# Kernel optimization log

Measured on AMD Instinct MI355X. Metric: run time of the kernel, lower is better.

## Reference

```python
import jax, jax.numpy as jnp
import numpy as np


def setup_inputs() -> dict:
    key = jax.random.key(0)
    ks = jax.random.split(key, 6)
    B, H, W, C = 4, 64, 64, 256
    D = 256 // 4  # inter_channel // 4
    return {
        "g": jax.random.normal(ks[0], (B, H, W, C), dtype=jnp.float32),
        "x": jax.random.normal(ks[1], (B, H, W, C), dtype=jnp.float32),
        "x_query": jax.random.normal(ks[2], (B, H, W, D), dtype=jnp.float32),
        "phi_g": jax.random.normal(ks[3], (B, H, W, D), dtype=jnp.float32),
        "x_value": jax.random.normal(ks[4], (B, H, W, C), dtype=jnp.float32),
        "k": jax.random.normal(ks[5], (1,), dtype=jnp.float32),
    }


def reference(g, x, x_query, phi_g, x_value, k):
    B, H, W, C = x.shape
    D = x_query.shape[-1]
    HW = H * W
    q = x_query.reshape(B, HW, D)
    pg = phi_g.reshape(B, HW, D)
    v = x_value.reshape(B, HW, C)
    # scale[b,i,j] = sum_d phi_g[b,i,d] * x_query[b,j,d]  -> (B, HW, HW)
    scale = jnp.einsum("bid,bjd->bij", pg, q)
    soft = jax.nn.softmax(scale, axis=-1)
    # scaled_value[b,i,c] = sum_j soft[b,i,j] * v[b,j,c]
    sv = jnp.einsum("bij,bjc->bic", soft, v).reshape(B, H, W, C)
    layero = k * sv + x
    return jnp.concatenate([layero, g], axis=3)
```

## Files before the change

kernel.cpp:

```cpp
#include <hip/hip_runtime.h>

#define N_  4096
#define D_  64
#define C_  256

typedef short bf16x8 __attribute__((ext_vector_type(8)));
typedef float f32x4  __attribute__((ext_vector_type(4)));

__device__ __forceinline__ unsigned short f2bf(float f) {
    union { float f; unsigned int i; } v; v.f = f;
    unsigned int r = v.i + 0x7fffu + ((v.i >> 16) & 1u);
    return (unsigned short)(r >> 16);
}

__global__ void prepass_kernel(const float* __restrict__ xq,
                               const float* __restrict__ pg,
                               const float* __restrict__ xv,
                               unsigned short* __restrict__ qbf,
                               unsigned short* __restrict__ pgbf,
                               unsigned short* __restrict__ vt2) {
    const int bid = blockIdx.x;
    const int t   = threadIdx.x;
    if (bid < 512) {
        const float* src = (bid < 256) ? xq : pg;
        unsigned short* dst = (bid < 256) ? qbf : pgbf;
        const int base = (bid & 255) * 1024 + t;
#pragma unroll
        for (int it = 0; it < 4; ++it) {
            const int i = base + it * 256;
            float4 v = ((const float4*)src)[i];
            ushort4 o;
            o.x = f2bf(v.x); o.y = f2bf(v.y); o.z = f2bf(v.z); o.w = f2bf(v.w);
            ((ushort4*)dst)[i] = o;
        }
        return;
    }
    const int lane = t & 63;
    const int w    = t >> 6;
    const int l15  = lane & 15;
    const int quad = lane >> 4;
    const int f    = (bid - 512) * 4 + w;
    const int b    = f >> 11;
    const int jt   = (f >> 6) & 31;
    const int cb   = (f >> 2) & 15;
    const int ks   = f & 3;
    const int c    = cb * 16 + l15;
    const int jb   = jt * 128 + ks * 32 + quad * 8;
    const float* src = xv + ((size_t)b * N_ + jb) * C_ + c;
    float v0 = src[0 * C_], v1 = src[1 * C_], v2 = src[2 * C_], v3 = src[3 * C_];
    float v4 = src[4 * C_], v5 = src[5 * C_], v6 = src[6 * C_], v7 = src[7 * C_];
    uint4 o;
    o.x = (unsigned)f2bf(v0) | ((unsigned)f2bf(v1) << 16);
    o.y = (unsigned)f2bf(v2) | ((unsigned)f2bf(v3) << 16);
    o.z = (unsigned)f2bf(v4) | ((unsigned)f2bf(v5) << 16);
    o.w = (unsigned)f2bf(v6) | ((unsigned)f2bf(v7) << 16);
    *(uint4*)(vt2 + (size_t)f * 512 + lane * 8) = o;
}

__global__ __launch_bounds__(512, 4) void attn_main(
    const float* __restrict__ g,  const float* __restrict__ x,
    const float* __restrict__ kk, float* __restrict__ out,
    const unsigned short* __restrict__ qbf,
    const unsigned short* __restrict__ pgbf,
    const unsigned short* __restrict__ vt2)
{
    __shared__ __align__(16) unsigned short p_lds[2][32][136];
    __shared__ float s_l[32];

    const int t    = threadIdx.x;
    const int lane = t & 63;
    const int w    = t >> 6;
    const int l15  = lane & 15;
    const int quad = lane >> 4;

    const int bid = blockIdx.x;
    const int b   = bid & 3;
    const int rg  = bid >> 2;
    const int i0  = rg * 32;
    const size_t rowbase = (size_t)b * N_ + i0;

    if (t < 32) s_l[t] = 0.f;

#pragma unroll
    for (int it = 0; it < 4; ++it) {
        const int row = it * 8 + w;
        const int c4  = lane * 4;
        const float4 gv = *(const float4*)(g + (rowbase + row) * C_ + c4);
        *(float4*)(out + (rowbase + row) * (2 * C_) + C_ + c4) = gv;
    }

    bf16x8 pgf[2][2];
#pragma unroll
    for (int mt = 0; mt < 2; ++mt)
#pragma unroll
        for (int ks = 0; ks < 2; ++ks)
            pgf[mt][ks] = *(const bf16x8*)(pgbf +
                (rowbase + mt * 16 + l15) * D_ + ks * 32 + quad * 8);

    f32x4 oacc[2][2];
#pragma unroll
    for (int mt = 0; mt < 2; ++mt) { oacc[mt][0] = (f32x4){0.f,0.f,0.f,0.f};
                                     oacc[mt][1] = (f32x4){0.f,0.f,0.f,0.f}; }
    float ls[2][4];
#pragma unroll
    for (int mt = 0; mt < 2; ++mt)
#pragma unroll
        for (int r = 0; r < 4; ++r) ls[mt][r] = 0.f;

    const unsigned short* qb  = qbf + (size_t)b * N_ * D_;
    const unsigned short* vtb = vt2 + (size_t)b * N_ * C_;

    bf16x8 qf[2];
#pragma unroll
    for (int ks = 0; ks < 2; ++ks)
        qf[ks] = *(const bf16x8*)(qb + (size_t)(w * 16 + l15) * D_ + ks * 32 + quad * 8);

    __syncthreads();

    for (int jt = 0; jt < 32; ++jt) {
        const int buf = jt & 1;
        const unsigned short* tbase = vtb + (size_t)jt * 32768;

        bf16x8 vf[4][2];
#pragma unroll
        for (int ks = 0; ks < 4; ++ks)
#pragma unroll
            for (int ctl = 0; ctl < 2; ++ctl)
                vf[ks][ctl] = *(const bf16x8*)(tbase +
                    (size_t)(((w * 2 + ctl) * 4) + ks) * 512 + lane * 8);

        f32x4 sacc[2];
#pragma unroll
        for (int mt = 0; mt < 2; ++mt) sacc[mt] = (f32x4){0.f,0.f,0.f,0.f};
#pragma unroll
        for (int ks = 0; ks < 2; ++ks)
#pragma unroll
            for (int mt = 0; mt < 2; ++mt)
                sacc[mt] = __builtin_amdgcn_mfma_f32_16x16x32_bf16(pgf[mt][ks], qf[ks], sacc[mt], 0, 0, 0);

#pragma unroll
        for (int mt = 0; mt < 2; ++mt)
#pragma unroll
            for (int r = 0; r < 4; ++r) {
                const float p = __expf(sacc[mt][r]);
                ls[mt][r] += p;
                p_lds[buf][mt * 16 + quad * 4 + r][w * 16 + l15] = f2bf(p);
            }
        __syncthreads();

        if (jt < 31) {
            const int jn = (jt + 1) * 128;
#pragma unroll
            for (int ks = 0; ks < 2; ++ks)
                qf[ks] = *(const bf16x8*)(qb +
                    (size_t)(jn + w * 16 + l15) * D_ + ks * 32 + quad * 8);
        }

#pragma unroll
        for (int ks = 0; ks < 4; ++ks) {
            bf16x8 pa[2];
#pragma unroll
            for (int mt = 0; mt < 2; ++mt)
                pa[mt] = *(const bf16x8*)&p_lds[buf][mt * 16 + l15][ks * 32 + quad * 8];
#pragma unroll
            for (int mt = 0; mt < 2; ++mt) {
                oacc[mt][0] = __builtin_amdgcn_mfma_f32_16x16x32_bf16(pa[mt], vf[ks][0], oacc[mt][0], 0, 0, 0);
                oacc[mt][1] = __builtin_amdgcn_mfma_f32_16x16x32_bf16(pa[mt], vf[ks][1], oacc[mt][1], 0, 0, 0);
            }
        }
    }

#pragma unroll
    for (int mt = 0; mt < 2; ++mt)
#pragma unroll
        for (int r = 0; r < 4; ++r) {
            float s = ls[mt][r];
            s += __shfl_xor(s, 1); s += __shfl_xor(s, 2);
            s += __shfl_xor(s, 4); s += __shfl_xor(s, 8);
            if (l15 == 0) atomicAdd(&s_l[mt * 16 + quad * 4 + r], s);
        }
    __syncthreads();

    const float kval = kk[0];
#pragma unroll
    for (int mt = 0; mt < 2; ++mt)
#pragma unroll
        for (int r = 0; r < 4; ++r) {
            const int m = mt * 16 + quad * 4 + r;
            const float linv = 1.f / s_l[m];
            const size_t row = rowbase + m;
#pragma unroll
            for (int ctl = 0; ctl < 2; ++ctl) {
                const int c = w * 32 + ctl * 16 + l15;
                out[row * (2 * C_) + c] = kval * (oacc[mt][ctl][r] * linv) + x[row * C_ + c];
            }
        }
}

#define ROWS 4
#define FNT  256
__global__ __launch_bounds__(FNT, 2) void attn_fallback(
    const float* __restrict__ g, const float* __restrict__ x,
    const float* __restrict__ xq, const float* __restrict__ pg,
    const float* __restrict__ xv, const float* __restrict__ kk,
    float* __restrict__ out)
{
    __shared__ __align__(16) float s_pg[ROWS][D_];
    __shared__ __align__(16) float s_sc[N_ * ROWS];
    __shared__ float s_rmax[4][ROWS];
    __shared__ float s_rsum[4][ROWS];

    const int t = threadIdx.x, lane = t & 63, w = t >> 6, blk = blockIdx.x;
    const int b = blk >> 10, i0 = (blk & 1023) * ROWS;
    const size_t rowbase = (size_t)b * N_ + i0;
    {
        const int r = t >> 6, cc = (t & 63) * 4;
        const float4 gv = *(const float4*)(g + (rowbase + r) * C_ + cc);
        *(float4*)(out + (rowbase + r) * (2 * C_) + C_ + cc) = gv;
    }
    { const int r = t >> 6, d = t & 63; s_pg[r][d] = pg[(rowbase + r) * D_ + d]; }
    __syncthreads();
    const float* qb = xq + (size_t)b * N_ * D_;
    float lmax[ROWS];
#pragma unroll
    for (int r = 0; r < ROWS; ++r) lmax[r] = -1e30f;
    for (int jj = 0; jj < N_ / FNT; ++jj) {
        const int j = t + jj * FNT;
        const float4* q4p = (const float4*)(qb + (size_t)j * D_);
        float s[ROWS] = {0.f, 0.f, 0.f, 0.f};
#pragma unroll
        for (int u = 0; u < D_ / 8; ++u) {
            const float4 qa = q4p[u * 2], qc = q4p[u * 2 + 1];
#pragma unroll
            for (int r = 0; r < ROWS; ++r) {
                const float4 pa = *(const float4*)&s_pg[r][u * 8];
                const float4 pb = *(const float4*)&s_pg[r][u * 8 + 4];
                s[r] += qa.x * pa.x + qa.y * pa.y + qa.z * pa.z + qa.w * pa.w
                      + qc.x * pb.x + qc.y * pb.y + qc.z * pb.z + qc.w * pb.w;
            }
        }
        *(float4*)&s_sc[j * ROWS] = make_float4(s[0], s[1], s[2], s[3]);
#pragma unroll
        for (int r = 0; r < ROWS; ++r) lmax[r] = fmaxf(lmax[r], s[r]);
    }
#pragma unroll
    for (int r = 0; r < ROWS; ++r) {
        float m = lmax[r];
        for (int o = 32; o > 0; o >>= 1) m = fmaxf(m, __shfl_down(m, o));
        if (lane == 0) s_rmax[w][r] = m;
    }
    __syncthreads();
    float bmax[ROWS];
#pragma unroll
    for (int r = 0; r < ROWS; ++r)
        bmax[r] = fmaxf(fmaxf(s_rmax[0][r], s_rmax[1][r]), fmaxf(s_rmax[2][r], s_rmax[3][r]));
    float lsum[ROWS] = {0.f, 0.f, 0.f, 0.f};
    for (int jj = 0; jj < N_ / FNT; ++jj) {
        const int j = t + jj * FNT;
        float4 s4 = *(const float4*)&s_sc[j * ROWS];
        s4.x = __expf(s4.x - bmax[0]); s4.y = __expf(s4.y - bmax[1]);
        s4.z = __expf(s4.z - bmax[2]); s4.w = __expf(s4.w - bmax[3]);
        *(float4*)&s_sc[j * ROWS] = s4;
        lsum[0] += s4.x; lsum[1] += s4.y; lsum[2] += s4.z; lsum[3] += s4.w;
    }
#pragma unroll
    for (int r = 0; r < ROWS; ++r) {
        float sm = lsum[r];
        for (int o = 32; o > 0; o >>= 1) sm += __shfl_down(sm, o);
        if (lane == 0) s_rsum[w][r] = sm;
    }
    __syncthreads();
    float rinv[ROWS];
#pragma unroll
    for (int r = 0; r < ROWS; ++r)
        rinv[r] = 1.f / (s_rsum[0][r] + s_rsum[1][r] + s_rsum[2][r] + s_rsum[3][r]);
    const int jg = lane >> 4;
    const int c0 = (w * 16 + (lane & 15)) * 4;
    const float* vb = xv + (size_t)b * N_ * C_;
    float acc[ROWS][4];
#pragma unroll
    for (int r = 0; r < ROWS; ++r)
#pragma unroll
        for (int q = 0; q < 4; ++q) acc[r][q] = 0.f;
#pragma unroll 4
    for (int jj = 0; jj < N_ / 4; ++jj) {
        const int j = jj * 4 + jg;
        const float4 p4 = *(const float4*)&s_sc[j * ROWS];
        const float4 v4 = *(const float4*)(vb + (size_t)j * C_ + c0);
        acc[0][0] += p4.x * v4.x; acc[0][1] += p4.x * v4.y; acc[0][2] += p4.x * v4.z; acc[0][3] += p4.x * v4.w;
        acc[1][0] += p4.y * v4.x; acc[1][1] += p4.y * v4.y; acc[1][2] += p4.y * v4.z; acc[1][3] += p4.y * v4.w;
        acc[2][0] += p4.z * v4.x; acc[2][1] += p4.z * v4.y; acc[2][2] += p4.z * v4.z; acc[2][3] += p4.z * v4.w;
        acc[3][0] += p4.w * v4.x; acc[3][1] += p4.w * v4.y; acc[3][2] += p4.w * v4.z; acc[3][3] += p4.w * v4.w;
    }
#pragma unroll
    for (int r = 0; r < ROWS; ++r)
#pragma unroll
        for (int q = 0; q < 4; ++q) {
            acc[r][q] += __shfl_xor(acc[r][q], 16);
            acc[r][q] += __shfl_xor(acc[r][q], 32);
        }
    const float kval = kk[0];
    if (lane < 16) {
        const int c = (w * 16 + lane) * 4;
#pragma unroll
        for (int r = 0; r < ROWS; ++r) {
            const float4 xv4 = *(const float4*)(x + (rowbase + r) * C_ + c);
            float4 ov;
            ov.x = kval * (acc[r][0] * rinv[r]) + xv4.x;
            ov.y = kval * (acc[r][1] * rinv[r]) + xv4.y;
            ov.z = kval * (acc[r][2] * rinv[r]) + xv4.z;
            ov.w = kval * (acc[r][3] * rinv[r]) + xv4.w;
            *(float4*)(out + (rowbase + r) * (2 * C_) + c) = ov;
        }
    }
}

extern "C" void kernel_launch(void* const* d_in, const int* in_sizes, int n_in,
                              void* d_out, int out_size, void* d_ws, size_t ws_size,
                              hipStream_t stream) {
    const float* g  = (const float*)d_in[0];
    const float* x  = (const float*)d_in[1];
    const float* xq = (const float*)d_in[2];
    const float* pg = (const float*)d_in[3];
    const float* xv = (const float*)d_in[4];
    const float* kk = (const float*)d_in[5];
    float* out = (float*)d_out;

    const int B = in_sizes[0] / (N_ * C_);
    const size_t qn = (size_t)B * N_ * D_;
    const size_t vn = (size_t)B * N_ * C_;
    const size_t need = (2 * qn + vn) * sizeof(unsigned short);

    if (B != 4 || ws_size < need) {
        attn_fallback<<<dim3(B * (N_ / ROWS)), FNT, 0, stream>>>(g, x, xq, pg, xv, kk, out);
        return;
    }

    unsigned short* qbf  = (unsigned short*)d_ws;
    unsigned short* pgbf = qbf + qn;
    unsigned short* vt2  = pgbf + qn;

    prepass_kernel<<<dim3(512 + B * 512), 256, 0, stream>>>(xq, pg, xv, qbf, pgbf, vt2);
    attn_main<<<dim3(B * (N_ / 32)), 512, 0, stream>>>(g, x, kk, out, qbf, pgbf, vt2);
}
```

Before: 174.6 us.

## Split attention along key dimension per wave with register P and LDS reduction

Restructures attn_main so each of 4 waves handles a disjoint slice of keys across all 256 output channels. Each wave computes P transposed directly into MFMA A-operand registers, so the per-tile LDS round trip and __syncthreads are gone. Partial outputs from the waves are combined through LDS at the end. This removes the per-iteration barrier and shared-memory traffic, but raises the accumulator register count to 128 floats per lane and reloads V fragments from global memory for every 32-key group.

```diff
diff --git a/kernel.cpp b/kernel.cpp
--- a/kernel.cpp
+++ b/kernel.cpp
@@ -57,14 +57,14 @@
     *(uint4*)(vt2 + (size_t)f * 512 + lane * 8) = o;
 }
 
-__global__ __launch_bounds__(512, 4) void attn_main(
+__global__ __launch_bounds__(256, 2) void attn_main(
     const float* __restrict__ g,  const float* __restrict__ x,
     const float* __restrict__ kk, float* __restrict__ out,
     const unsigned short* __restrict__ qbf,
     const unsigned short* __restrict__ pgbf,
     const unsigned short* __restrict__ vt2)
 {
-    __shared__ __align__(16) unsigned short p_lds[2][32][136];
+    __shared__ float s_o[2][C_][36];
     __shared__ float s_l[32];
 
     const int t    = threadIdx.x;
@@ -80,121 +80,131 @@
     const size_t rowbase = (size_t)b * N_ + i0;
 
     if (t < 32) s_l[t] = 0.f;
-
-#pragma unroll
-    for (int it = 0; it < 4; ++it) {
-        const int row = it * 8 + w;
-        const int c4  = lane * 4;
-        const float4 gv = *(const float4*)(g + (rowbase + row) * C_ + c4);
-        *(float4*)(out + (rowbase + row) * (2 * C_) + C_ + c4) = gv;
+    __syncthreads();
+
+#pragma unroll
+    for (int it = 0; it < 8; ++it) {
+        const int row = it * 4 + w;
+        const float4 gv = *(const float4*)(g + (rowbase + row) * C_ + lane * 4);
+        *(float4*)(out + (rowbase + row) * (2 * C_) + C_ + lane * 4) = gv;
     }
 
     bf16x8 pgf[2][2];
 #pragma unroll
-    for (int mt = 0; mt < 2; ++mt)
+    for (int nt = 0; nt < 2; ++nt)
 #pragma unroll
         for (int ks = 0; ks < 2; ++ks)
-            pgf[mt][ks] = *(const bf16x8*)(pgbf +
-                (rowbase + mt * 16 + l15) * D_ + ks * 32 + quad * 8);
-
-    f32x4 oacc[2][2];
-#pragma unroll
-    for (int mt = 0; mt < 2; ++mt) { oacc[mt][0] = (f32x4){0.f,0.f,0.f,0.f};
-                                     oacc[mt][1] = (f32x4){0.f,0.f,0.f,0.f}; }
-    float ls[2][4];
-#pragma unroll
-    for (int mt = 0; mt < 2; ++mt)
-#pragma unroll
-        for (int r = 0; r < 4; ++r) ls[mt][r] = 0.f;
+            pgf[nt][ks] = *(const bf16x8*)(pgbf +
+                (rowbase + nt * 16 + l15) * D_ + ks * 32 + quad * 8);
+
+    f32x4 oacc[2][16];
+#pragma unroll
+    for (int nt = 0; nt < 2; ++nt)
+#pragma unroll
+        for (int ct = 0; ct < 16; ++ct)
+            oacc[nt][ct] = (f32x4){0.f, 0.f, 0.f, 0.f};
+
+    float ls[2] = {0.f, 0.f};
 
     const unsigned short* qb  = qbf + (size_t)b * N_ * D_;
     const unsigned short* vtb = vt2 + (size_t)b * N_ * C_;
 
-    bf16x8 qf[2];
-#pragma unroll
-    for (int ks = 0; ks < 2; ++ks)
-        qf[ks] = *(const bf16x8*)(qb + (size_t)(w * 16 + l15) * D_ + ks * 32 + quad * 8);
-
-    __syncthreads();
-
-    for (int jt = 0; jt < 32; ++jt) {
-        const int buf = jt & 1;
-        const unsigned short* tbase = vtb + (size_t)jt * 32768;
-
-        bf16x8 vf[4][2];
-#pragma unroll
-        for (int ks = 0; ks < 4; ++ks)
-#pragma unroll
-            for (int ctl = 0; ctl < 2; ++ctl)
-                vf[ks][ctl] = *(const bf16x8*)(tbase +
-                    (size_t)(((w * 2 + ctl) * 4) + ks) * 512 + lane * 8);
-
-        f32x4 sacc[2];
-#pragma unroll
-        for (int mt = 0; mt < 2; ++mt) sacc[mt] = (f32x4){0.f,0.f,0.f,0.f};
-#pragma unroll
-        for (int ks = 0; ks < 2; ++ks)
-#pragma unroll
-            for (int mt = 0; mt < 2; ++mt)
-                sacc[mt] = __builtin_amdgcn_mfma_f32_16x16x32_bf16(pgf[mt][ks], qf[ks], sacc[mt], 0, 0, 0);
-
-#pragma unroll
-        for (int mt = 0; mt < 2; ++mt)
-#pragma unroll
-            for (int r = 0; r < 4; ++r) {
-                const float p = __expf(sacc[mt][r]);
-                ls[mt][r] += p;
-                p_lds[buf][mt * 16 + quad * 4 + r][w * 16 + l15] = f2bf(p);
+    const int jperm = 8 * (l15 >> 2) + (l15 & 3);
+
+    for (int iter = 0; iter < 16; ++iter) {
+        const int j0 = iter * 256 + w * 64;
+#pragma unroll
+        for (int kg = 0; kg < 2; ++kg) {
+            const int jg0 = j0 + kg * 32;
+
+            bf16x8 qf[2][2];
+#pragma unroll
+            for (int tt = 0; tt < 2; ++tt)
+#pragma unroll
+                for (int ks = 0; ks < 2; ++ks)
+                    qf[tt][ks] = *(const bf16x8*)(qb +
+                        (size_t)(jg0 + 4 * tt + jperm) * D_ + ks * 32 + quad * 8);
+
+            f32x4 sacc[2][2];
+#pragma unroll
+            for (int tt = 0; tt < 2; ++tt) { sacc[tt][0] = (f32x4){0.f,0.f,0.f,0.f};
+                                             sacc[tt][1] = (f32x4){0.f,0.f,0.f,0.f}; }
+#pragma unroll
+            for (int ks = 0; ks < 2; ++ks)
+#pragma unroll
+                for (int tt = 0; tt < 2; ++tt)
+#pragma unroll
+                    for (int nt = 0; nt < 2; ++nt)
+                        sacc[tt][nt] = __builtin_amdgcn_mfma_f32_16x16x32_bf16(
+                            qf[tt][ks], pgf[nt][ks], sacc[tt][nt], 0, 0, 0);
+
+            union { unsigned int u[4]; bf16x8 h; } pa[2];
+#pragma unroll
+            for (int nt = 0; nt < 2; ++nt)
+#pragma unroll
+                for (int tt = 0; tt < 2; ++tt)
+#pragma unroll
+                    for (int rp = 0; rp < 2; ++rp) {
+                        const float pA = __expf(sacc[tt][nt][2 * rp]);
+                        const float pB = __expf(sacc[tt][nt][2 * rp + 1]);
+                        ls[nt] += pA + pB;
+                        pa[nt].u[tt * 2 + rp] =
+                            (unsigned)f2bf(pA) | ((unsigned)f2bf(pB) << 16);
+                    }
+
+            const int jt128 = jg0 >> 7;
+            const int kssel = (jg0 >> 5) & 3;
+            const unsigned short* fb = vtb +
+                ((size_t)(jt128 * 16) * 4 + kssel) * 512 + (size_t)lane * 8;
+#pragma unroll
+            for (int ct = 0; ct < 16; ++ct) {
+                const bf16x8 vf = *(const bf16x8*)(fb + (size_t)ct * 2048);
+                oacc[0][ct] = __builtin_amdgcn_mfma_f32_16x16x32_bf16(pa[0].h, vf, oacc[0][ct], 0, 0, 0);
+                oacc[1][ct] = __builtin_amdgcn_mfma_f32_16x16x32_bf16(pa[1].h, vf, oacc[1][ct], 0, 0, 0);
             }
-        __syncthreads();
-
-        if (jt < 31) {
-            const int jn = (jt + 1) * 128;
-#pragma unroll
-            for (int ks = 0; ks < 2; ++ks)
-                qf[ks] = *(const bf16x8*)(qb +
-                    (size_t)(jn + w * 16 + l15) * D_ + ks * 32 + quad * 8);
-        }
-
-#pragma unroll
-        for (int ks = 0; ks < 4; ++ks) {
-            bf16x8 pa[2];
-#pragma unroll
-            for (int mt = 0; mt < 2; ++mt)
-                pa[mt] = *(const bf16x8*)&p_lds[buf][mt * 16 + l15][ks * 32 + quad * 8];
-#pragma unroll
-            for (int mt = 0; mt < 2; ++mt) {
-                oacc[mt][0] = __builtin_amdgcn_mfma_f32_16x16x32_bf16(pa[mt], vf[ks][0], oacc[mt][0], 0, 0, 0);
-                oacc[mt][1] = __builtin_amdgcn_mfma_f32_16x16x32_bf16(pa[mt], vf[ks][1], oacc[mt][1], 0, 0, 0);
+        }
+    }
+
+#pragma unroll
+    for (int nt = 0; nt < 2; ++nt) {
+        float s = ls[nt];
+        s += __shfl_xor(s, 16);
+        s += __shfl_xor(s, 32);
+        if (lane < 16) atomicAdd(&s_l[nt * 16 + lane], s);
+    }
+
+    if (w >= 2) {
+        float* r = &s_o[w - 2][0][0];
+#pragma unroll
+        for (int nt = 0; nt < 2; ++nt)
+#pragma unroll
+            for (int ct = 0; ct < 16; ++ct)
+                *(f32x4*)&r[(ct * 16 + l15) * 36 + nt * 16 + 4 * quad] = oacc[nt][ct];
+    }
+    __syncthreads();
+    if (w < 2) {
+        float* r = &s_o[w][0][0];
+#pragma unroll
+        for (int nt = 0; nt < 2; ++nt)
+#pragma unroll
+            for (int ct = 0; ct < 16; ++ct) {
+                const int idx = (ct * 16 + l15) * 36 + nt * 16 + 4 * quad;
+                f32x4 v = *(f32x4*)&r[idx];
+                v += oacc[nt][ct];
+                *(f32x4*)&r[idx] = v;
             }
-        }
-    }
-
-#pragma unroll
-    for (int mt = 0; mt < 2; ++mt)
-#pragma unroll
-        for (int r = 0; r < 4; ++r) {
-            float s = ls[mt][r];
-            s += __shfl_xor(s, 1); s += __shfl_xor(s, 2);
-            s += __shfl_xor(s, 4); s += __shfl_xor(s, 8);
-            if (l15 == 0) atomicAdd(&s_l[mt * 16 + quad * 4 + r], s);
-        }
+    }
     __syncthreads();
 
     const float kval = kk[0];
-#pragma unroll
-    for (int mt = 0; mt < 2; ++mt)
-#pragma unroll
-        for (int r = 0; r < 4; ++r) {
-            const int m = mt * 16 + quad * 4 + r;
-            const float linv = 1.f / s_l[m];
-            const size_t row = rowbase + m;
-#pragma unroll
-            for (int ctl = 0; ctl < 2; ++ctl) {
-                const int c = w * 32 + ctl * 16 + l15;
-                out[row * (2 * C_) + c] = kval * (oacc[mt][ctl][r] * linv) + x[row * C_ + c];
-            }
-        }
+    const int c = t;
+#pragma unroll 4
+    for (int row = 0; row < 32; ++row) {
+        const float linv = 1.f / s_l[row];
+        const float oe = s_o[0][c][row] + s_o[1][c][row];
+        const size_t rr = rowbase + row;
+        out[rr * (2 * C_) + c] = kval * (oe * linv) + x[rr * C_ + c];
+    }
 }
 
 #define ROWS 4
@@ -341,5 +351,5 @@
     unsigned short* vt2  = pgbf + qn;
 
     prepass_kernel<<<dim3(512 + B * 512), 256, 0, stream>>>(xq, pg, xv, qbf, pgbf, vt2);
-    attn_main<<<dim3(B * (N_ / 32)), 512, 0, stream>>>(g, x, kk, out, qbf, pgbf, vt2);
-}
+    attn_main<<<dim3(B * (N_ / 32)), 256, 0, stream>>>(g, x, kk, out, qbf, pgbf, vt2);
+}
```

Result: slower. 250.6 us (+43.6%).
